# Optimization experiments

Measured on AMD Instinct MI355X. Metric: run time of the kernel, lower is better.

Reference implementation:

```python
import jax, jax.numpy as jnp
import numpy as np

B, S, H = 2, 1024, 4096
NH, NKV, HD = 32, 8, 128
GROUPS = NH // NKV  # num_key_value_groups
ROPE_THETA = 10000.0


def setup_inputs() -> dict:
    key = jax.random.key(0)
    k0, k1, k2 = jax.random.split(key, 3)
    x = jax.random.normal(k0, (B, S, H), jnp.float32)
    w_qkv = jax.random.normal(k1, (H, (NH + 2 * NKV) * HD), jnp.float32) * (1.0 / np.sqrt(H))
    w_o = jax.random.normal(k2, (NH * HD, H), jnp.float32) * (1.0 / np.sqrt(H))
    # rotary cos/sin tables (llama freqs_cis, interleaved-pair convention)
    inv_freq = 1.0 / (ROPE_THETA ** (np.arange(0, HD, 2, dtype=np.float64) / HD))
    freqs = np.outer(np.arange(S, dtype=np.float64), inv_freq)  # [S, HD/2]
    cos = jnp.asarray(np.cos(freqs), jnp.float32)
    sin = jnp.asarray(np.sin(freqs), jnp.float32)
    # additive causal mask [1,1,S,S]
    causal = np.tril(np.ones((S, S), dtype=bool))
    mask = jnp.asarray(np.where(causal, 0.0, -1e9), jnp.float32)[None, None]
    return {"x": x, "w_qkv": w_qkv, "w_o": w_o, "cos": cos, "sin": sin, "mask": mask}


def _rope(t, cos, sin):
    # t: [B,S,N,HD]; rotate interleaved (even, odd) pairs like complex mult by freqs_cis
    t2 = t.reshape(t.shape[:-1] + (HD // 2, 2))
    t0, t1 = t2[..., 0], t2[..., 1]
    c = cos[None, :, None, :]  # [1,S,1,HD/2]
    s = sin[None, :, None, :]
    r0 = t0 * c - t1 * s
    r1 = t0 * s + t1 * c
    return jnp.stack([r0, r1], axis=-1).reshape(t.shape)


def reference(x, w_qkv, w_o, cos, sin, mask):
    b, s, _ = x.shape
    xqkv = (x @ w_qkv).reshape(b, s, NH + 2 * NKV, HD)
    xq = xqkv[:, :, :NH]                  # [b,s,NH,HD]
    xk = xqkv[:, :, NH:NH + NKV]          # [b,s,NKV,HD]
    xv = xqkv[:, :, NH + NKV:]            # [b,s,NKV,HD]
    xq = _rope(xq, cos, sin)
    xk = _rope(xk, cos, sin)
    # GQA: repeat kv heads to match query heads (repeat_interleave on head dim)
    k = jnp.repeat(xk, GROUPS, axis=2)
    v = jnp.repeat(xv, GROUPS, axis=2)
    scores = jnp.einsum('bqhd,bkhd->bhqk', xq, k) / np.float32(np.sqrt(HD))
    scores = scores + mask
    probs = jax.nn.softmax(scores.astype(jnp.float32), axis=-1).astype(xq.dtype)
    out = jnp.einsum('bhqk,bkhd->bqhd', probs, v).reshape(b, s, NH * HD)
    return out @ w_o
```

## Files before the change

kernel.cpp:

```cpp
#include <hip/hip_runtime.h>
#include <cstdint>
#include <cstddef>

typedef short bf16x8 __attribute__((ext_vector_type(8)));
typedef float f32x4 __attribute__((ext_vector_type(4)));

__device__ __forceinline__ unsigned short f2bf(float f) {
  unsigned int u = __builtin_bit_cast(unsigned int, f);
  u += 0x7fffu + ((u >> 16) & 1u);
  return (unsigned short)(u >> 16);
}

__device__ __forceinline__ void transpose_tile(const float* __restrict__ src,
                                               unsigned short* __restrict__ dst,
                                               int K, int N, int n0, int k0, int tid,
                                               float* __restrict__ tb ) {
#pragma unroll
  for (int i = 0; i < 4; ++i) {
    const int lr = tid >> 4, lc = (tid & 15) * 4;
    float4 v = *(const float4*)(src + (size_t)(k0 + i * 16 + lr) * N + n0 + lc);
    tb[(i * 16 + lr) * 65 + lc] = v.x;
    tb[(i * 16 + lr) * 65 + lc + 1] = v.y;
    tb[(i * 16 + lr) * 65 + lc + 2] = v.z;
    tb[(i * 16 + lr) * 65 + lc + 3] = v.w;
  }
  __syncthreads();
  const int nr = tid >> 3, kk = (tid & 7) * 8;
#pragma unroll
  for (int i = 0; i < 2; ++i) {
    int n = nr + i * 32;
    bf16x8 v;
#pragma unroll
    for (int j = 0; j < 8; ++j) v[j] = (short)f2bf(tb[(kk + j) * 65 + n]);
    *(bf16x8*)(dst + (size_t)(n0 + n) * K + k0 + kk) = v;
  }
}

__global__ __launch_bounds__(256) void k_prep(const float* __restrict__ x,
                                              const float* __restrict__ w_qkv,
                                              unsigned short* __restrict__ xb,
                                              unsigned short* __restrict__ wqkv_t) {
  __shared__ float tb[64 * 65];
  const int bid = blockIdx.x, tid = threadIdx.x;
  if (bid < 8192) {
    int i = bid * 256 + tid;
    float4 v = ((const float4*)x)[i];
    ushort4 o;
    o.x = f2bf(v.x); o.y = f2bf(v.y); o.z = f2bf(v.z); o.w = f2bf(v.w);
    ((ushort4*)xb)[i] = o;
  } else {
    int t = bid - 8192;
    transpose_tile(w_qkv, wqkv_t, 4096, 6144, (t % 96) * 64, (t / 96) * 64, tid, tb);
  }
}

template <int MODE>
__global__ __launch_bounds__(256) void k_gemm(const unsigned short* __restrict__ A,
                                              const unsigned short* __restrict__ Bt,
                                              float* __restrict__ C,
                                              unsigned short* __restrict__ Qr,
                                              unsigned short* __restrict__ Kr,
                                              unsigned short* __restrict__ Vt,
                                              const float* __restrict__ cosT,
                                              const float* __restrict__ sinT,
                                              const float* __restrict__ w_o,
                                              unsigned short* __restrict__ wo_t,
                                              int M, int N, int K) {
  __shared__ __align__(16) char smem[32768];
  unsigned short* lA = (unsigned short*)smem;
  unsigned short* lB = (unsigned short*)(smem + 16384);
  const int tid = threadIdx.x;

  int bm, bn;
  if (MODE == 1) {
    const int bid = blockIdx.x;
    if (bid >= 768) {
      int t = bid - 768;
      transpose_tile(w_o, wo_t, 4096, 4096, (t & 63) * 64, (t >> 6) * 64, tid, (float*)smem);
      return;
    }
    const int swz = (bid & 7) * 96 + (bid >> 3);
    bm = (swz & 15) * 128;
    bn = (swz >> 4) * 128;
  } else {
    const int lid = blockIdx.y * gridDim.x + blockIdx.x;
    const int cpx = (gridDim.x * gridDim.y) >> 3;
    const int swz = (lid & 7) * cpx + (lid >> 3);
    bm = (swz % gridDim.x) * 128;
    bn = (swz / gridDim.x) * 128;
  }

  const int lane = tid & 63, wv = tid >> 6;
  const int wr = wv >> 1, wc = wv & 1;
  const int l16 = lane & 15, lhi = lane >> 4;
  f32x4 acc[4][4] = {};
  bf16x8 ar[4], br[4];

#pragma unroll
  for (int i = 0; i < 4; ++i) {
    int c = tid + i * 256, row = c >> 3, c16 = c & 7;
    ar[i] = *(const bf16x8*)(A + (size_t)(bm + row) * K + 0 + c16 * 8);
    br[i] = *(const bf16x8*)(Bt + (size_t)(bn + row) * K + 0 + c16 * 8);
  }
  const int nkt = K >> 6;
  for (int kt = 0; kt < nkt; ++kt) {
    __syncthreads();
#pragma unroll
    for (int i = 0; i < 4; ++i) {
      int c = tid + i * 256, row = c >> 3, c16 = c & 7;
      int pc = c16 ^ (row & 7);
      *(bf16x8*)((char*)lA + row * 128 + pc * 16) = ar[i];
      *(bf16x8*)((char*)lB + row * 128 + pc * 16) = br[i];
    }
    __syncthreads();
    if (kt + 1 < nkt) {
      int kofs = (kt + 1) << 6;
#pragma unroll
      for (int i = 0; i < 4; ++i) {
        int c = tid + i * 256, row = c >> 3, c16 = c & 7;
        ar[i] = *(const bf16x8*)(A + (size_t)(bm + row) * K + kofs + c16 * 8);
        br[i] = *(const bf16x8*)(Bt + (size_t)(bn + row) * K + kofs + c16 * 8);
      }
    }
#pragma unroll
    for (int s = 0; s < 2; ++s) {
      bf16x8 af[4], bfr[4];
#pragma unroll
      for (int f = 0; f < 4; ++f) {
        int rowa = wr * 64 + f * 16 + l16;
        int ca = (s * 4 + lhi) ^ (rowa & 7);
        af[f] = *(const bf16x8*)((char*)lA + rowa * 128 + ca * 16);
        int rowb = wc * 64 + f * 16 + l16;
        int cb = (s * 4 + lhi) ^ (rowb & 7);
        bfr[f] = *(const bf16x8*)((char*)lB + rowb * 128 + cb * 16);
      }
#pragma unroll
      for (int fi = 0; fi < 4; ++fi)
#pragma unroll
        for (int fj = 0; fj < 4; ++fj)
          acc[fi][fj] = __builtin_amdgcn_mfma_f32_16x16x32_bf16(af[fi], bfr[fj], acc[fi][fj], 0, 0, 0);
    }
  }

  if (MODE == 0) {
#pragma unroll
    for (int fi = 0; fi < 4; ++fi) {
      int rbase = bm + wr * 64 + fi * 16 + lhi * 4;
#pragma unroll
      for (int fj = 0; fj < 4; ++fj) {
        int col = bn + wc * 64 + fj * 16 + l16;
#pragma unroll
        for (int r = 0; r < 4; ++r)
          C[(size_t)(rbase + r) * N + col] = acc[fi][fj][r];
      }
    }
  } else {
#pragma unroll
    for (int fi = 0; fi < 4; ++fi) {
      int rbase = bm + wr * 64 + fi * 16 + lhi * 4;
      int b = rbase >> 10, sbase = rbase & 1023;
#pragma unroll
      for (int fj = 0; fj < 4; ++fj) {
        int col = bn + wc * 64 + fj * 16 + l16;
        if (col < 5120) {
          int i = (col & 127) >> 1;
          float sgn = (col & 1) ? 1.0f : -1.0f;
          unsigned short* dst;
          if (col < 4096)
            dst = Qr + ((size_t)(b * 32 + (col >> 7)) * 1024) * 128 + (col & 127);
          else
            dst = Kr + ((size_t)(b * 8 + ((col - 4096) >> 7)) * 1024) * 128 + (col & 127);
#pragma unroll
          for (int r = 0; r < 4; ++r) {
            float own = acc[fi][fj][r];
            float other = __shfl_xor(own, 1);
            int s = sbase + r;
            float c = cosT[s * 64 + i], sn = sinT[s * 64 + i];
            dst[(size_t)s * 128] = f2bf(own * c + sgn * other * sn);
          }
        } else {
          int kvh = (col - 5120) >> 7, d = col & 127;
          unsigned short* dst = Vt + ((size_t)(b * 8 + kvh) * 128 + d) * 1024;
#pragma unroll
          for (int r = 0; r < 4; ++r) dst[sbase + r] = f2bf(acc[fi][fj][r]);
        }
      }
    }
  }
}

__global__ __launch_bounds__(256) void k_attn(const unsigned short* __restrict__ Qr,
                                              const unsigned short* __restrict__ Kr,
                                              const unsigned short* __restrict__ Vt,
                                              unsigned short* __restrict__ Out) {
  __shared__ __align__(16) unsigned short lK[64 * 128];
  __shared__ __align__(16) unsigned short lV[128 * 64];
  __shared__ __align__(16) unsigned short lP[4 * 16 * 64];
  const int tid = threadIdx.x, lane = tid & 63, wv = tid >> 6;
  const int qt = (int)gridDim.x - 1 - (int)blockIdx.x;
  const int h = blockIdx.y, b = blockIdx.z;
  const int kvh = h >> 2;
  const int q0 = qt * 64;
  const int l16 = lane & 15, lhi = lane >> 4;

  const unsigned short* Qbase = Qr + ((size_t)(b * 32 + h) * 1024 + q0 + wv * 16 + l16) * 128;
  bf16x8 qf[4];
#pragma unroll
  for (int s = 0; s < 4; ++s) qf[s] = *(const bf16x8*)(Qbase + s * 32 + lhi * 8);

  const unsigned short* Kbase = Kr + (size_t)(b * 8 + kvh) * 1024 * 128;
  const unsigned short* Vbase = Vt + (size_t)(b * 8 + kvh) * 128 * 1024;

  f32x4 oacc[8] = {};
  float mrow[4] = {-1e30f, -1e30f, -1e30f, -1e30f};
  float lrow[4] = {0.f, 0.f, 0.f, 0.f};
  const int ntk = qt + 1;
  bf16x8 kreg[4], vreg[4];

#pragma unroll
  for (int i = 0; i < 4; ++i) {
    int c = tid + i * 256;
    int krow = c >> 4, kc = c & 15;
    kreg[i] = *(const bf16x8*)(Kbase + (size_t)krow * 128 + kc * 8);
    int vrow = c >> 3, vc = c & 7;
    vreg[i] = *(const bf16x8*)(Vbase + (size_t)vrow * 1024 + vc * 8);
  }

  for (int kt = 0; kt < ntk; ++kt) {
    const int k0 = kt * 64;
    __syncthreads();
#pragma unroll
    for (int i = 0; i < 4; ++i) {
      int c = tid + i * 256;
      int krow = c >> 4, kc = c & 15;
      *(bf16x8*)((char*)lK + krow * 256 + (kc ^ (krow & 7)) * 16) = kreg[i];
      int vrow = c >> 3, vc = c & 7;
      *(bf16x8*)((char*)lV + vrow * 128 + (vc ^ (vrow & 7)) * 16) = vreg[i];
    }
    __syncthreads();

    if (kt + 1 < ntk) {
      const int kn = (kt + 1) * 64;
#pragma unroll
      for (int i = 0; i < 4; ++i) {
        int c = tid + i * 256;
        int krow = c >> 4, kc = c & 15;
        kreg[i] = *(const bf16x8*)(Kbase + (size_t)(kn + krow) * 128 + kc * 8);
        int vrow = c >> 3, vc = c & 7;
        vreg[i] = *(const bf16x8*)(Vbase + (size_t)vrow * 1024 + kn + vc * 8);
      }
    }

    f32x4 sacc[4] = {};
#pragma unroll
    for (int kf = 0; kf < 4; ++kf) {
      int rowk = kf * 16 + l16;
#pragma unroll
      for (int s = 0; s < 4; ++s) {
        int ck = (s * 4 + lhi) ^ (rowk & 7);
        bf16x8 kfr = *(const bf16x8*)((char*)lK + rowk * 256 + ck * 16);
        sacc[kf] = __builtin_amdgcn_mfma_f32_16x16x32_bf16(qf[s], kfr, sacc[kf], 0, 0, 0);
      }
    }

    const int qg = q0 + wv * 16 + lhi * 4;
    float mt[4] = {-1e30f, -1e30f, -1e30f, -1e30f};
#pragma unroll
    for (int kf = 0; kf < 4; ++kf) {
      int kg = k0 + kf * 16 + l16;
#pragma unroll
      for (int r = 0; r < 4; ++r) {
        float v = sacc[kf][r] * 0.08838834764831845f;
        v = (kg <= qg + r) ? v : -1e9f;
        sacc[kf][r] = v;
        mt[r] = fmaxf(mt[r], v);
      }
    }
#pragma unroll
    for (int r = 0; r < 4; ++r) {
#pragma unroll
      for (int off = 1; off < 16; off <<= 1) mt[r] = fmaxf(mt[r], __shfl_xor(mt[r], off));
    }

    bool need = false;
#pragma unroll
    for (int r = 0; r < 4; ++r) need = need || (mt[r] > mrow[r] + 8.0f);
    const bool doresc = (__ballot(need) != 0ull);

    float alpha[4], rs[4];
#pragma unroll
    for (int r = 0; r < 4; ++r) {
      if (doresc) {
        float mn = fmaxf(mrow[r], mt[r]);
        alpha[r] = __expf(mrow[r] - mn);
        mrow[r] = mn;
      } else {
        alpha[r] = 1.0f;
      }
      rs[r] = 0.f;
    }
#pragma unroll
    for (int kf = 0; kf < 4; ++kf) {
      int key = kf * 16 + l16;
#pragma unroll
      for (int r = 0; r < 4; ++r) {
        float p = __expf(sacc[kf][r] - mrow[r]);
        rs[r] += p;
        int prow = lhi * 4 + r;
        int addr = wv * 2048 + ((prow * 128 + key * 2) ^ ((prow & 7) << 4));
        *(unsigned short*)((char*)lP + addr) = f2bf(p);
      }
    }
#pragma unroll
    for (int r = 0; r < 4; ++r) {
#pragma unroll
      for (int off = 1; off < 16; off <<= 1) rs[r] += __shfl_xor(rs[r], off);
      lrow[r] = lrow[r] * alpha[r] + rs[r];
    }
    if (doresc) {
#pragma unroll
      for (int nf = 0; nf < 8; ++nf)
#pragma unroll
        for (int r = 0; r < 4; ++r) oacc[nf][r] *= alpha[r];
    }

#pragma unroll
    for (int s2 = 0; s2 < 2; ++s2) {
      int prow = l16;
      int paddr = wv * 2048 + ((prow * 128 + s2 * 64 + lhi * 16) ^ ((prow & 7) << 4));
      bf16x8 pa = *(const bf16x8*)((char*)lP + paddr);
#pragma unroll
      for (int nf = 0; nf < 8; ++nf) {
        int rowd = nf * 16 + l16;
        int cv = (s2 * 4 + lhi) ^ (rowd & 7);
        bf16x8 vfr = *(const bf16x8*)((char*)lV + rowd * 128 + cv * 16);
        oacc[nf] = __builtin_amdgcn_mfma_f32_16x16x32_bf16(pa, vfr, oacc[nf], 0, 0, 0);
      }
    }
  }

  unsigned short* Ob = Out + ((size_t)(b * 1024) + q0 + wv * 16 + lhi * 4) * 4096 + h * 128;
#pragma unroll
  for (int r = 0; r < 4; ++r) {
    float inv = 1.f / lrow[r];
#pragma unroll
    for (int nf = 0; nf < 8; ++nf)
      Ob[(size_t)r * 4096 + nf * 16 + l16] = f2bf(oacc[nf][r] * inv);
  }
}

extern "C" void kernel_launch(void* const* d_in, const int* in_sizes, int n_in,
                              void* d_out, int out_size, void* d_ws, size_t ws_size,
                              hipStream_t stream) {
  const float* x = (const float*)d_in[0];
  const float* w_qkv = (const float*)d_in[1];
  const float* w_o = (const float*)d_in[2];
  const float* cosT = (const float*)d_in[3];
  const float* sinT = (const float*)d_in[4];

  char* ws = (char*)d_ws;
  unsigned short* wqkv_t = (unsigned short*)(ws);
  unsigned short* wo_t   = (unsigned short*)(ws + 50331648);
  unsigned short* xb     = (unsigned short*)(ws + 83886080);
  unsigned short* Qr     = (unsigned short*)(ws + 100663296);
  unsigned short* Kr     = (unsigned short*)(ws + 117440512);
  unsigned short* Vt     = (unsigned short*)(ws + 121634816);
  unsigned short* attn   = (unsigned short*)(ws + 125829120);

  k_prep<<<14336, 256, 0, stream>>>(x, w_qkv, xb, wqkv_t);
  k_gemm<1><<<768 + 4096, 256, 0, stream>>>(xb, wqkv_t, nullptr, Qr, Kr, Vt, cosT, sinT,
                                            w_o, wo_t, 2048, 6144, 4096);
  k_attn<<<dim3(16, 32, 2), 256, 0, stream>>>(Qr, Kr, Vt, attn);
  k_gemm<0><<<dim3(16, 32), 256, 0, stream>>>(attn, wo_t, (float*)d_out, nullptr, nullptr, nullptr,
                                              nullptr, nullptr, nullptr, nullptr, 2048, 4096, 4096);
}
```

Baseline: 318.8 us.

## Fuse all stages into one cooperative persistent kernel with grid syncs

Replaces the four-kernel pipeline with a single cooperative kernel of 768 blocks. It runs prep, the QKV GEMM with RoPE, attention and the output GEMM in sequence, separated by grid.sync. Attention work is load-balanced by pairing each causal tile with its complement, and the w_o transpose fills the idle blocks during the attention phase. This removes launch gaps and hides the w_o transpose, but adds grid-barrier cost, a per-call host occupancy query and properties lookup, and leaves a third of the blocks idle in the final GEMM. The old multi-kernel path is kept as a fallback.

```diff
diff --git a/kernel.cpp b/kernel.cpp
--- a/kernel.cpp
+++ b/kernel.cpp
@@ -1,6 +1,9 @@
 #include <hip/hip_runtime.h>
+#include <hip/hip_cooperative_groups.h>
 #include <cstdint>
 #include <cstddef>
+
+namespace cg = cooperative_groups;
 
 typedef short bf16x8 __attribute__((ext_vector_type(8)));
 typedef float f32x4 __attribute__((ext_vector_type(4)));
@@ -33,6 +36,353 @@
 #pragma unroll
     for (int j = 0; j < 8; ++j) v[j] = (short)f2bf(tb[(kk + j) * 65 + n]);
     *(bf16x8*)(dst + (size_t)(n0 + n) * K + k0 + kk) = v;
+  }
+}
+
+__device__ __forceinline__ void gemm_core(const unsigned short* __restrict__ A,
+                                          const unsigned short* __restrict__ Bt,
+                                          int K, int bm, int bn, int tid,
+                                          unsigned short* __restrict__ lA,
+                                          unsigned short* __restrict__ lB,
+                                          f32x4 (&acc)[4][4]) {
+  const int lane = tid & 63, wv = tid >> 6;
+  const int wr = wv >> 1, wc = wv & 1;
+  const int l16 = lane & 15, lhi = lane >> 4;
+  bf16x8 ar[4], br[4];
+#pragma unroll
+  for (int i = 0; i < 4; ++i) {
+    int c = tid + i * 256, row = c >> 3, c16 = c & 7;
+    ar[i] = *(const bf16x8*)(A + (size_t)(bm + row) * K + 0 + c16 * 8);
+    br[i] = *(const bf16x8*)(Bt + (size_t)(bn + row) * K + 0 + c16 * 8);
+  }
+  const int nkt = K >> 6;
+  for (int kt = 0; kt < nkt; ++kt) {
+    __syncthreads();
+#pragma unroll
+    for (int i = 0; i < 4; ++i) {
+      int c = tid + i * 256, row = c >> 3, c16 = c & 7;
+      int pc = c16 ^ (row & 7);
+      *(bf16x8*)((char*)lA + row * 128 + pc * 16) = ar[i];
+      *(bf16x8*)((char*)lB + row * 128 + pc * 16) = br[i];
+    }
+    __syncthreads();
+    if (kt + 1 < nkt) {
+      int kofs = (kt + 1) << 6;
+#pragma unroll
+      for (int i = 0; i < 4; ++i) {
+        int c = tid + i * 256, row = c >> 3, c16 = c & 7;
+        ar[i] = *(const bf16x8*)(A + (size_t)(bm + row) * K + kofs + c16 * 8);
+        br[i] = *(const bf16x8*)(Bt + (size_t)(bn + row) * K + kofs + c16 * 8);
+      }
+    }
+#pragma unroll
+    for (int s = 0; s < 2; ++s) {
+      bf16x8 af[4], bfr[4];
+#pragma unroll
+      for (int f = 0; f < 4; ++f) {
+        int rowa = wr * 64 + f * 16 + l16;
+        int ca = (s * 4 + lhi) ^ (rowa & 7);
+        af[f] = *(const bf16x8*)((char*)lA + rowa * 128 + ca * 16);
+        int rowb = wc * 64 + f * 16 + l16;
+        int cb = (s * 4 + lhi) ^ (rowb & 7);
+        bfr[f] = *(const bf16x8*)((char*)lB + rowb * 128 + cb * 16);
+      }
+#pragma unroll
+      for (int fi = 0; fi < 4; ++fi)
+#pragma unroll
+        for (int fj = 0; fj < 4; ++fj)
+          acc[fi][fj] = __builtin_amdgcn_mfma_f32_16x16x32_bf16(af[fi], bfr[fj], acc[fi][fj], 0, 0, 0);
+    }
+  }
+}
+
+__device__ __forceinline__ void qkv_epilogue(f32x4 (&acc)[4][4], int bm, int bn, int tid,
+                                             unsigned short* __restrict__ Qr,
+                                             unsigned short* __restrict__ Kr,
+                                             unsigned short* __restrict__ Vt,
+                                             const float* __restrict__ cosT,
+                                             const float* __restrict__ sinT) {
+  const int lane = tid & 63, wv = tid >> 6;
+  const int wr = wv >> 1, wc = wv & 1;
+  const int l16 = lane & 15, lhi = lane >> 4;
+#pragma unroll
+  for (int fi = 0; fi < 4; ++fi) {
+    int rbase = bm + wr * 64 + fi * 16 + lhi * 4;
+    int b = rbase >> 10, sbase = rbase & 1023;
+#pragma unroll
+    for (int fj = 0; fj < 4; ++fj) {
+      int col = bn + wc * 64 + fj * 16 + l16;
+      if (col < 5120) {
+        int ip = (col & 127) >> 1;
+        float sgn = (col & 1) ? 1.0f : -1.0f;
+        unsigned short* dst;
+        if (col < 4096)
+          dst = Qr + ((size_t)(b * 32 + (col >> 7)) * 1024) * 128 + (col & 127);
+        else
+          dst = Kr + ((size_t)(b * 8 + ((col - 4096) >> 7)) * 1024) * 128 + (col & 127);
+#pragma unroll
+        for (int r = 0; r < 4; ++r) {
+          float own = acc[fi][fj][r];
+          float other = __shfl_xor(own, 1);
+          int s = sbase + r;
+          float c = cosT[s * 64 + ip], sn = sinT[s * 64 + ip];
+          dst[(size_t)s * 128] = f2bf(own * c + sgn * other * sn);
+        }
+      } else {
+        int kvh = (col - 5120) >> 7, d = col & 127;
+        unsigned short* dst = Vt + ((size_t)(b * 8 + kvh) * 128 + d) * 1024;
+#pragma unroll
+        for (int r = 0; r < 4; ++r) dst[sbase + r] = f2bf(acc[fi][fj][r]);
+      }
+    }
+  }
+}
+
+__device__ __forceinline__ void attn_tile(const unsigned short* __restrict__ Qr,
+                                          const unsigned short* __restrict__ Kr,
+                                          const unsigned short* __restrict__ Vt,
+                                          unsigned short* __restrict__ Out,
+                                          int qt, int h, int b, int tid,
+                                          unsigned short* __restrict__ lK,
+                                          unsigned short* __restrict__ lV,
+                                          unsigned short* __restrict__ lP) {
+  const int lane = tid & 63, wv = tid >> 6;
+  const int kvh = h >> 2;
+  const int q0 = qt * 64;
+  const int l16 = lane & 15, lhi = lane >> 4;
+
+  const unsigned short* Qbase = Qr + ((size_t)(b * 32 + h) * 1024 + q0 + wv * 16 + l16) * 128;
+  bf16x8 qf[4];
+#pragma unroll
+  for (int s = 0; s < 4; ++s) qf[s] = *(const bf16x8*)(Qbase + s * 32 + lhi * 8);
+
+  const unsigned short* Kbase = Kr + (size_t)(b * 8 + kvh) * 1024 * 128;
+  const unsigned short* Vbase = Vt + (size_t)(b * 8 + kvh) * 128 * 1024;
+
+  f32x4 oacc[8] = {};
+  float mrow[4] = {-1e30f, -1e30f, -1e30f, -1e30f};
+  float lrow[4] = {0.f, 0.f, 0.f, 0.f};
+  const int ntk = qt + 1;
+  bf16x8 kreg[4], vreg[4];
+
+#pragma unroll
+  for (int i = 0; i < 4; ++i) {
+    int c = tid + i * 256;
+    int krow = c >> 4, kc = c & 15;
+    kreg[i] = *(const bf16x8*)(Kbase + (size_t)krow * 128 + kc * 8);
+    int vrow = c >> 3, vc = c & 7;
+    vreg[i] = *(const bf16x8*)(Vbase + (size_t)vrow * 1024 + vc * 8);
+  }
+
+  for (int kt = 0; kt < ntk; ++kt) {
+    const int k0 = kt * 64;
+    __syncthreads();
+#pragma unroll
+    for (int i = 0; i < 4; ++i) {
+      int c = tid + i * 256;
+      int krow = c >> 4, kc = c & 15;
+      *(bf16x8*)((char*)lK + krow * 256 + (kc ^ (krow & 7)) * 16) = kreg[i];
+      int vrow = c >> 3, vc = c & 7;
+      *(bf16x8*)((char*)lV + vrow * 128 + (vc ^ (vrow & 7)) * 16) = vreg[i];
+    }
+    __syncthreads();
+
+    if (kt + 1 < ntk) {
+      const int kn = (kt + 1) * 64;
+#pragma unroll
+      for (int i = 0; i < 4; ++i) {
+        int c = tid + i * 256;
+        int krow = c >> 4, kc = c & 15;
+        kreg[i] = *(const bf16x8*)(Kbase + (size_t)(kn + krow) * 128 + kc * 8);
+        int vrow = c >> 3, vc = c & 7;
+        vreg[i] = *(const bf16x8*)(Vbase + (size_t)vrow * 1024 + kn + vc * 8);
+      }
+    }
+
+    f32x4 sacc[4] = {};
+#pragma unroll
+    for (int kf = 0; kf < 4; ++kf) {
+      int rowk = kf * 16 + l16;
+#pragma unroll
+      for (int s = 0; s < 4; ++s) {
+        int ck = (s * 4 + lhi) ^ (rowk & 7);
+        bf16x8 kfr = *(const bf16x8*)((char*)lK + rowk * 256 + ck * 16);
+        sacc[kf] = __builtin_amdgcn_mfma_f32_16x16x32_bf16(qf[s], kfr, sacc[kf], 0, 0, 0);
+      }
+    }
+
+    const int qg = q0 + wv * 16 + lhi * 4;
+    float mt[4] = {-1e30f, -1e30f, -1e30f, -1e30f};
+#pragma unroll
+    for (int kf = 0; kf < 4; ++kf) {
+      int kg = k0 + kf * 16 + l16;
+#pragma unroll
+      for (int r = 0; r < 4; ++r) {
+        float v = sacc[kf][r] * 0.08838834764831845f;
+        v = (kg <= qg + r) ? v : -1e9f;
+        sacc[kf][r] = v;
+        mt[r] = fmaxf(mt[r], v);
+      }
+    }
+#pragma unroll
+    for (int r = 0; r < 4; ++r) {
+#pragma unroll
+      for (int off = 1; off < 16; off <<= 1) mt[r] = fmaxf(mt[r], __shfl_xor(mt[r], off));
+    }
+
+    bool need = false;
+#pragma unroll
+    for (int r = 0; r < 4; ++r) need = need || (mt[r] > mrow[r] + 8.0f);
+    const bool doresc = (__ballot(need) != 0ull);
+
+    float alpha[4], rs[4];
+#pragma unroll
+    for (int r = 0; r < 4; ++r) {
+      if (doresc) {
+        float mn = fmaxf(mrow[r], mt[r]);
+        alpha[r] = __expf(mrow[r] - mn);
+        mrow[r] = mn;
+      } else {
+        alpha[r] = 1.0f;
+      }
+      rs[r] = 0.f;
+    }
+#pragma unroll
+    for (int kf = 0; kf < 4; ++kf) {
+      int key = kf * 16 + l16;
+#pragma unroll
+      for (int r = 0; r < 4; ++r) {
+        float p = __expf(sacc[kf][r] - mrow[r]);
+        rs[r] += p;
+        int prow = lhi * 4 + r;
+        int addr = wv * 2048 + ((prow * 128 + key * 2) ^ ((prow & 7) << 4));
+        *(unsigned short*)((char*)lP + addr) = f2bf(p);
+      }
+    }
+#pragma unroll
+    for (int r = 0; r < 4; ++r) {
+#pragma unroll
+      for (int off = 1; off < 16; off <<= 1) rs[r] += __shfl_xor(rs[r], off);
+      lrow[r] = lrow[r] * alpha[r] + rs[r];
+    }
+    if (doresc) {
+#pragma unroll
+      for (int nf = 0; nf < 8; ++nf)
+#pragma unroll
+        for (int r = 0; r < 4; ++r) oacc[nf][r] *= alpha[r];
+    }
+
+#pragma unroll
+    for (int s2 = 0; s2 < 2; ++s2) {
+      int prow = l16;
+      int paddr = wv * 2048 + ((prow * 128 + s2 * 64 + lhi * 16) ^ ((prow & 7) << 4));
+      bf16x8 pa = *(const bf16x8*)((char*)lP + paddr);
+#pragma unroll
+      for (int nf = 0; nf < 8; ++nf) {
+        int rowd = nf * 16 + l16;
+        int cv = (s2 * 4 + lhi) ^ (rowd & 7);
+        bf16x8 vfr = *(const bf16x8*)((char*)lV + rowd * 128 + cv * 16);
+        oacc[nf] = __builtin_amdgcn_mfma_f32_16x16x32_bf16(pa, vfr, oacc[nf], 0, 0, 0);
+      }
+    }
+  }
+
+  unsigned short* Ob = Out + ((size_t)(b * 1024) + q0 + wv * 16 + lhi * 4) * 4096 + h * 128;
+#pragma unroll
+  for (int r = 0; r < 4; ++r) {
+    float inv = 1.f / lrow[r];
+#pragma unroll
+    for (int nf = 0; nf < 8; ++nf)
+      Ob[(size_t)r * 4096 + nf * 16 + l16] = f2bf(oacc[nf][r] * inv);
+  }
+}
+
+__global__ __launch_bounds__(256, 3) void k_mega(
+    const float* __restrict__ x, const float* __restrict__ w_qkv,
+    const float* __restrict__ w_o, const float* __restrict__ cosT,
+    const float* __restrict__ sinT, unsigned short* __restrict__ xb,
+    unsigned short* __restrict__ wqkv_t, unsigned short* __restrict__ wo_t,
+    unsigned short* __restrict__ Qr, unsigned short* __restrict__ Kr,
+    unsigned short* __restrict__ Vt, unsigned short* __restrict__ attnO,
+    float* __restrict__ outp) {
+  __shared__ __align__(16) char smem[40960];
+  cg::grid_group grid = cg::this_grid();
+  const int bid = blockIdx.x, tid = threadIdx.x;
+
+  for (int it = bid; it < 14336; it += 768) {
+    if (it < 8192) {
+      int i = it * 256 + tid;
+      float4 v = ((const float4*)x)[i];
+      ushort4 o;
+      o.x = f2bf(v.x); o.y = f2bf(v.y); o.z = f2bf(v.z); o.w = f2bf(v.w);
+      ((ushort4*)xb)[i] = o;
+    } else {
+      int t = it - 8192;
+      __syncthreads();
+      transpose_tile(w_qkv, wqkv_t, 4096, 6144, (t % 96) * 64, (t / 96) * 64, tid, (float*)smem);
+    }
+  }
+  __threadfence();
+  grid.sync();
+
+  {
+    unsigned short* lA = (unsigned short*)smem;
+    unsigned short* lB = (unsigned short*)(smem + 16384);
+    const int swz = (bid & 7) * 96 + (bid >> 3);
+    const int bm = (swz & 15) * 128, bn = (swz >> 4) * 128;
+    f32x4 acc[4][4] = {};
+    gemm_core(xb, wqkv_t, 4096, bm, bn, tid, lA, lB, acc);
+    qkv_epilogue(acc, bm, bn, tid, Qr, Kr, Vt, cosT, sinT);
+  }
+  __threadfence();
+  grid.sync();
+
+  {
+    unsigned short* lK = (unsigned short*)smem;
+    unsigned short* lV = (unsigned short*)(smem + 16384);
+    unsigned short* lP = (unsigned short*)(smem + 32768);
+    int t1 = bid;
+    attn_tile(Qr, Kr, Vt, attnO, t1 & 15, (t1 >> 4) & 31, t1 >> 9, tid, lK, lV, lP);
+    if (bid < 256) {
+      int t2 = 1023 - bid;
+      attn_tile(Qr, Kr, Vt, attnO, t2 & 15, (t2 >> 4) & 31, t2 >> 9, tid, lK, lV, lP);
+    } else {
+      int g = (bid - 256) >> 4, a = bid & 15;
+      int t0 = g * 136 + 16 * a - (a * (a - 1)) / 2;
+      int cnt = 16 - a;
+      for (int j = 0; j < cnt; ++j) {
+        int t = t0 + j;
+        if (t < 4096) {
+          __syncthreads();
+          transpose_tile(w_o, wo_t, 4096, 4096, (t & 63) * 64, (t >> 6) * 64, tid, (float*)smem);
+        }
+      }
+    }
+  }
+  __threadfence();
+  grid.sync();
+
+  if (bid < 512) {
+    unsigned short* lA = (unsigned short*)smem;
+    unsigned short* lB = (unsigned short*)(smem + 16384);
+    const int swz = (bid & 7) * 64 + (bid >> 3);
+    const int bm = (swz & 15) * 128, bn = (swz >> 4) * 128;
+    f32x4 acc[4][4] = {};
+    gemm_core(attnO, wo_t, 4096, bm, bn, tid, lA, lB, acc);
+    const int lane = tid & 63, wv = tid >> 6;
+    const int wr = wv >> 1, wc = wv & 1;
+    const int l16 = lane & 15, lhi = lane >> 4;
+#pragma unroll
+    for (int fi = 0; fi < 4; ++fi) {
+      int rbase = bm + wr * 64 + fi * 16 + lhi * 4;
+#pragma unroll
+      for (int fj = 0; fj < 4; ++fj) {
+        int col = bn + wc * 64 + fj * 16 + l16;
+#pragma unroll
+        for (int r = 0; r < 4; ++r)
+          outp[(size_t)(rbase + r) * 4096 + col] = acc[fi][fj][r];
+      }
+    }
   }
 }
 
@@ -54,298 +404,68 @@
   }
 }
 
-template <int MODE>
-__global__ __launch_bounds__(256) void k_gemm(const unsigned short* __restrict__ A,
-                                              const unsigned short* __restrict__ Bt,
-                                              float* __restrict__ C,
-                                              unsigned short* __restrict__ Qr,
-                                              unsigned short* __restrict__ Kr,
-                                              unsigned short* __restrict__ Vt,
-                                              const float* __restrict__ cosT,
-                                              const float* __restrict__ sinT,
-                                              const float* __restrict__ w_o,
-                                              unsigned short* __restrict__ wo_t,
-                                              int M, int N, int K) {
+__global__ __launch_bounds__(256) void k_qkv(const unsigned short* __restrict__ A,
+                                             const unsigned short* __restrict__ Bt,
+                                             unsigned short* __restrict__ Qr,
+                                             unsigned short* __restrict__ Kr,
+                                             unsigned short* __restrict__ Vt,
+                                             const float* __restrict__ cosT,
+                                             const float* __restrict__ sinT,
+                                             const float* __restrict__ w_o,
+                                             unsigned short* __restrict__ wo_t) {
+  __shared__ __align__(16) char smem[32768];
+  const int bid = blockIdx.x, tid = threadIdx.x;
+  if (bid >= 768) {
+    int t = bid - 768;
+    transpose_tile(w_o, wo_t, 4096, 4096, (t & 63) * 64, (t >> 6) * 64, tid, (float*)smem);
+    return;
+  }
+  unsigned short* lA = (unsigned short*)smem;
+  unsigned short* lB = (unsigned short*)(smem + 16384);
+  const int swz = (bid & 7) * 96 + (bid >> 3);
+  const int bm = (swz & 15) * 128, bn = (swz >> 4) * 128;
+  f32x4 acc[4][4] = {};
+  gemm_core(A, Bt, 4096, bm, bn, tid, lA, lB, acc);
+  qkv_epilogue(acc, bm, bn, tid, Qr, Kr, Vt, cosT, sinT);
+}
+
+__global__ __launch_bounds__(256) void k_attn(const unsigned short* __restrict__ Qr,
+                                              const unsigned short* __restrict__ Kr,
+                                              const unsigned short* __restrict__ Vt,
+                                              unsigned short* __restrict__ Out) {
+  __shared__ __align__(16) char smem[40960];
+  unsigned short* lK = (unsigned short*)smem;
+  unsigned short* lV = (unsigned short*)(smem + 16384);
+  unsigned short* lP = (unsigned short*)(smem + 32768);
+  const int qt = (int)gridDim.x - 1 - (int)blockIdx.x;
+  attn_tile(Qr, Kr, Vt, Out, qt, blockIdx.y, blockIdx.z, threadIdx.x, lK, lV, lP);
+}
+
+__global__ __launch_bounds__(256) void k_out(const unsigned short* __restrict__ A,
+                                             const unsigned short* __restrict__ Bt,
+                                             float* __restrict__ C) {
   __shared__ __align__(16) char smem[32768];
   unsigned short* lA = (unsigned short*)smem;
   unsigned short* lB = (unsigned short*)(smem + 16384);
   const int tid = threadIdx.x;
-
-  int bm, bn;
-  if (MODE == 1) {
-    const int bid = blockIdx.x;
-    if (bid >= 768) {
-      int t = bid - 768;
-      transpose_tile(w_o, wo_t, 4096, 4096, (t & 63) * 64, (t >> 6) * 64, tid, (float*)smem);
-      return;
-    }
-    const int swz = (bid & 7) * 96 + (bid >> 3);
-    bm = (swz & 15) * 128;
-    bn = (swz >> 4) * 128;
-  } else {
-    const int lid = blockIdx.y * gridDim.x + blockIdx.x;
-    const int cpx = (gridDim.x * gridDim.y) >> 3;
-    const int swz = (lid & 7) * cpx + (lid >> 3);
-    bm = (swz % gridDim.x) * 128;
-    bn = (swz / gridDim.x) * 128;
-  }
-
+  const int lid = blockIdx.y * gridDim.x + blockIdx.x;
+  const int swz = (lid & 7) * 64 + (lid >> 3);
+  const int bm = (swz & 15) * 128, bn = (swz >> 4) * 128;
+  f32x4 acc[4][4] = {};
+  gemm_core(A, Bt, 4096, bm, bn, tid, lA, lB, acc);
   const int lane = tid & 63, wv = tid >> 6;
   const int wr = wv >> 1, wc = wv & 1;
   const int l16 = lane & 15, lhi = lane >> 4;
-  f32x4 acc[4][4] = {};
-  bf16x8 ar[4], br[4];
-
-#pragma unroll
-  for (int i = 0; i < 4; ++i) {
-    int c = tid + i * 256, row = c >> 3, c16 = c & 7;
-    ar[i] = *(const bf16x8*)(A + (size_t)(bm + row) * K + 0 + c16 * 8);
-    br[i] = *(const bf16x8*)(Bt + (size_t)(bn + row) * K + 0 + c16 * 8);
-  }
-  const int nkt = K >> 6;
-  for (int kt = 0; kt < nkt; ++kt) {
-    __syncthreads();
-#pragma unroll
-    for (int i = 0; i < 4; ++i) {
-      int c = tid + i * 256, row = c >> 3, c16 = c & 7;
-      int pc = c16 ^ (row & 7);
-      *(bf16x8*)((char*)lA + row * 128 + pc * 16) = ar[i];
-      *(bf16x8*)((char*)lB + row * 128 + pc * 16) = br[i];
-    }
-    __syncthreads();
-    if (kt + 1 < nkt) {
-      int kofs = (kt + 1) << 6;
-#pragma unroll
-      for (int i = 0; i < 4; ++i) {
-        int c = tid + i * 256, row = c >> 3, c16 = c & 7;
-        ar[i] = *(const bf16x8*)(A + (size_t)(bm + row) * K + kofs + c16 * 8);
-        br[i] = *(const bf16x8*)(Bt + (size_t)(bn + row) * K + kofs + c16 * 8);
-      }
-    }
-#pragma unroll
-    for (int s = 0; s < 2; ++s) {
-      bf16x8 af[4], bfr[4];
-#pragma unroll
-      for (int f = 0; f < 4; ++f) {
-        int rowa = wr * 64 + f * 16 + l16;
-        int ca = (s * 4 + lhi) ^ (rowa & 7);
-        af[f] = *(const bf16x8*)((char*)lA + rowa * 128 + ca * 16);
-        int rowb = wc * 64 + f * 16 + l16;
-        int cb = (s * 4 + lhi) ^ (rowb & 7);
-        bfr[f] = *(const bf16x8*)((char*)lB + rowb * 128 + cb * 16);
-      }
-#pragma unroll
-      for (int fi = 0; fi < 4; ++fi)
-#pragma unroll
-        for (int fj = 0; fj < 4; ++fj)
-          acc[fi][fj] = __builtin_amdgcn_mfma_f32_16x16x32_bf16(af[fi], bfr[fj], acc[fi][fj], 0, 0, 0);
-    }
-  }
-
-  if (MODE == 0) {
-#pragma unroll
-    for (int fi = 0; fi < 4; ++fi) {
-      int rbase = bm + wr * 64 + fi * 16 + lhi * 4;
-#pragma unroll
-      for (int fj = 0; fj < 4; ++fj) {
-        int col = bn + wc * 64 + fj * 16 + l16;
-#pragma unroll
-        for (int r = 0; r < 4; ++r)
-          C[(size_t)(rbase + r) * N + col] = acc[fi][fj][r];
-      }
-    }
-  } else {
-#pragma unroll
-    for (int fi = 0; fi < 4; ++fi) {
-      int rbase = bm + wr * 64 + fi * 16 + lhi * 4;
-      int b = rbase >> 10, sbase = rbase & 1023;
-#pragma unroll
-      for (int fj = 0; fj < 4; ++fj) {
-        int col = bn + wc * 64 + fj * 16 + l16;
-        if (col < 5120) {
-          int i = (col & 127) >> 1;
-          float sgn = (col & 1) ? 1.0f : -1.0f;
-          unsigned short* dst;
-          if (col < 4096)
-            dst = Qr + ((size_t)(b * 32 + (col >> 7)) * 1024) * 128 + (col & 127);
-          else
-            dst = Kr + ((size_t)(b * 8 + ((col - 4096) >> 7)) * 1024) * 128 + (col & 127);
-#pragma unroll
-          for (int r = 0; r < 4; ++r) {
-            float own = acc[fi][fj][r];
-            float other = __shfl_xor(own, 1);
-            int s = sbase + r;
-            float c = cosT[s * 64 + i], sn = sinT[s * 64 + i];
-            dst[(size_t)s * 128] = f2bf(own * c + sgn * other * sn);
-          }
-        } else {
-          int kvh = (col - 5120) >> 7, d = col & 127;
-          unsigned short* dst = Vt + ((size_t)(b * 8 + kvh) * 128 + d) * 1024;
-#pragma unroll
-          for (int r = 0; r < 4; ++r) dst[sbase + r] = f2bf(acc[fi][fj][r]);
-        }
-      }
-    }
-  }
-}
-
-__global__ __launch_bounds__(256) void k_attn(const unsigned short* __restrict__ Qr,
-                                              const unsigned short* __restrict__ Kr,
-                                              const unsigned short* __restrict__ Vt,
-                                              unsigned short* __restrict__ Out) {
-  __shared__ __align__(16) unsigned short lK[64 * 128];
-  __shared__ __align__(16) unsigned short lV[128 * 64];
-  __shared__ __align__(16) unsigned short lP[4 * 16 * 64];
-  const int tid = threadIdx.x, lane = tid & 63, wv = tid >> 6;
-  const int qt = (int)gridDim.x - 1 - (int)blockIdx.x;
-  const int h = blockIdx.y, b = blockIdx.z;
-  const int kvh = h >> 2;
-  const int q0 = qt * 64;
-  const int l16 = lane & 15, lhi = lane >> 4;
-
-  const unsigned short* Qbase = Qr + ((size_t)(b * 32 + h) * 1024 + q0 + wv * 16 + l16) * 128;
-  bf16x8 qf[4];
-#pragma unroll
-  for (int s = 0; s < 4; ++s) qf[s] = *(const bf16x8*)(Qbase + s * 32 + lhi * 8);
-
-  const unsigned short* Kbase = Kr + (size_t)(b * 8 + kvh) * 1024 * 128;
-  const unsigned short* Vbase = Vt + (size_t)(b * 8 + kvh) * 128 * 1024;
-
-  f32x4 oacc[8] = {};
-  float mrow[4] = {-1e30f, -1e30f, -1e30f, -1e30f};
-  float lrow[4] = {0.f, 0.f, 0.f, 0.f};
-  const int ntk = qt + 1;
-  bf16x8 kreg[4], vreg[4];
-
-#pragma unroll
-  for (int i = 0; i < 4; ++i) {
-    int c = tid + i * 256;
-    int krow = c >> 4, kc = c & 15;
-    kreg[i] = *(const bf16x8*)(Kbase + (size_t)krow * 128 + kc * 8);
-    int vrow = c >> 3, vc = c & 7;
-    vreg[i] = *(const bf16x8*)(Vbase + (size_t)vrow * 1024 + vc * 8);
-  }
-
-  for (int kt = 0; kt < ntk; ++kt) {
-    const int k0 = kt * 64;
-    __syncthreads();
-#pragma unroll
-    for (int i = 0; i < 4; ++i) {
-      int c = tid + i * 256;
-      int krow = c >> 4, kc = c & 15;
-      *(bf16x8*)((char*)lK + krow * 256 + (kc ^ (krow & 7)) * 16) = kreg[i];
-      int vrow = c >> 3, vc = c & 7;
-      *(bf16x8*)((char*)lV + vrow * 128 + (vc ^ (vrow & 7)) * 16) = vreg[i];
-    }
-    __syncthreads();
-
-    if (kt + 1 < ntk) {
-      const int kn = (kt + 1) * 64;
-#pragma unroll
-      for (int i = 0; i < 4; ++i) {
-        int c = tid + i * 256;
-        int krow = c >> 4, kc = c & 15;
-        kreg[i] = *(const bf16x8*)(Kbase + (size_t)(kn + krow) * 128 + kc * 8);
-        int vrow = c >> 3, vc = c & 7;
-        vreg[i] = *(const bf16x8*)(Vbase + (size_t)vrow * 1024 + kn + vc * 8);
-      }
-    }
-
-    f32x4 sacc[4] = {};
-#pragma unroll
-    for (int kf = 0; kf < 4; ++kf) {
-      int rowk = kf * 16 + l16;
-#pragma unroll
-      for (int s = 0; s < 4; ++s) {
-        int ck = (s * 4 + lhi) ^ (rowk & 7);
-        bf16x8 kfr = *(const bf16x8*)((char*)lK + rowk * 256 + ck * 16);
-        sacc[kf] = __builtin_amdgcn_mfma_f32_16x16x32_bf16(qf[s], kfr, sacc[kf], 0, 0, 0);
-      }
-    }
-
-    const int qg = q0 + wv * 16 + lhi * 4;
-    float mt[4] = {-1e30f, -1e30f, -1e30f, -1e30f};
-#pragma unroll
-    for (int kf = 0; kf < 4; ++kf) {
-      int kg = k0 + kf * 16 + l16;
-#pragma unroll
-      for (int r = 0; r < 4; ++r) {
-        float v = sacc[kf][r] * 0.08838834764831845f;
-        v = (kg <= qg + r) ? v : -1e9f;
-        sacc[kf][r] = v;
-        mt[r] = fmaxf(mt[r], v);
-      }
-    }
-#pragma unroll
-    for (int r = 0; r < 4; ++r) {
-#pragma unroll
-      for (int off = 1; off < 16; off <<= 1) mt[r] = fmaxf(mt[r], __shfl_xor(mt[r], off));
-    }
-
-    bool need = false;
-#pragma unroll
-    for (int r = 0; r < 4; ++r) need = need || (mt[r] > mrow[r] + 8.0f);
-    const bool doresc = (__ballot(need) != 0ull);
-
-    float alpha[4], rs[4];
-#pragma unroll
-    for (int r = 0; r < 4; ++r) {
-      if (doresc) {
-        float mn = fmaxf(mrow[r], mt[r]);
-        alpha[r] = __expf(mrow[r] - mn);
-        mrow[r] = mn;
-      } else {
-        alpha[r] = 1.0f;
-      }
-      rs[r] = 0.f;
-    }
-#pragma unroll
-    for (int kf = 0; kf < 4; ++kf) {
-      int key = kf * 16 + l16;
-#pragma unroll
-      for (int r = 0; r < 4; ++r) {
-        float p = __expf(sacc[kf][r] - mrow[r]);
-        rs[r] += p;
-        int prow = lhi * 4 + r;
-        int addr = wv * 2048 + ((prow * 128 + key * 2) ^ ((prow & 7) << 4));
-        *(unsigned short*)((char*)lP + addr) = f2bf(p);
-      }
-    }
-#pragma unroll
-    for (int r = 0; r < 4; ++r) {
-#pragma unroll
-      for (int off = 1; off < 16; off <<= 1) rs[r] += __shfl_xor(rs[r], off);
-      lrow[r] = lrow[r] * alpha[r] + rs[r];
-    }
-    if (doresc) {
-#pragma unroll
-      for (int nf = 0; nf < 8; ++nf)
-#pragma unroll
-        for (int r = 0; r < 4; ++r) oacc[nf][r] *= alpha[r];
-    }
-
-#pragma unroll
-    for (int s2 = 0; s2 < 2; ++s2) {
-      int prow = l16;
-      int paddr = wv * 2048 + ((prow * 128 + s2 * 64 + lhi * 16) ^ ((prow & 7) << 4));
-      bf16x8 pa = *(const bf16x8*)((char*)lP + paddr);
-#pragma unroll
-      for (int nf = 0; nf < 8; ++nf) {
-        int rowd = nf * 16 + l16;
-        int cv = (s2 * 4 + lhi) ^ (rowd & 7);
-        bf16x8 vfr = *(const bf16x8*)((char*)lV + rowd * 128 + cv * 16);
-        oacc[nf] = __builtin_amdgcn_mfma_f32_16x16x32_bf16(pa, vfr, oacc[nf], 0, 0, 0);
-      }
-    }
-  }
-
-  unsigned short* Ob = Out + ((size_t)(b * 1024) + q0 + wv * 16 + lhi * 4) * 4096 + h * 128;
-#pragma unroll
-  for (int r = 0; r < 4; ++r) {
-    float inv = 1.f / lrow[r];
-#pragma unroll
-    for (int nf = 0; nf < 8; ++nf)
-      Ob[(size_t)r * 4096 + nf * 16 + l16] = f2bf(oacc[nf][r] * inv);
+#pragma unroll
+  for (int fi = 0; fi < 4; ++fi) {
+    int rbase = bm + wr * 64 + fi * 16 + lhi * 4;
+#pragma unroll
+    for (int fj = 0; fj < 4; ++fj) {
+      int col = bn + wc * 64 + fj * 16 + l16;
+#pragma unroll
+      for (int r = 0; r < 4; ++r)
+        C[(size_t)(rbase + r) * 4096 + col] = acc[fi][fj][r];
+    }
   }
 }
 
@@ -366,11 +486,26 @@
   unsigned short* Kr     = (unsigned short*)(ws + 117440512);
   unsigned short* Vt     = (unsigned short*)(ws + 121634816);
   unsigned short* attn   = (unsigned short*)(ws + 125829120);
+  float* outp = (float*)d_out;
+
+  int dev = 0;
+  hipGetDevice(&dev);
+  hipDeviceProp_t prop;
+  hipGetDeviceProperties(&prop, dev);
+  int nb = 0;
+  hipOccupancyMaxActiveBlocksPerMultiprocessor(&nb, k_mega, 256, 0);
+  bool coop = (prop.cooperativeLaunch != 0) && (nb * prop.multiProcessorCount >= 768);
+
+  if (coop) {
+    void* args[] = {&x, &w_qkv, &w_o, &cosT, &sinT, &xb, &wqkv_t, &wo_t,
+                    &Qr, &Kr, &Vt, &attn, &outp};
+    hipError_t e = hipLaunchCooperativeKernel((const void*)k_mega, dim3(768), dim3(256),
+                                              args, 0, stream);
+    if (e == hipSuccess) return;
+  }
 
   k_prep<<<14336, 256, 0, stream>>>(x, w_qkv, xb, wqkv_t);
-  k_gemm<1><<<768 + 4096, 256, 0, stream>>>(xb, wqkv_t, nullptr, Qr, Kr, Vt, cosT, sinT,
-                                            w_o, wo_t, 2048, 6144, 4096);
+  k_qkv<<<768 + 4096, 256, 0, stream>>>(xb, wqkv_t, Qr, Kr, Vt, cosT, sinT, w_o, wo_t);
   k_attn<<<dim3(16, 32, 2), 256, 0, stream>>>(Qr, Kr, Vt, attn);
-  k_gemm<0><<<dim3(16, 32), 256, 0, stream>>>(attn, wo_t, (float*)d_out, nullptr, nullptr, nullptr,
-                                              nullptr, nullptr, nullptr, nullptr, 2048, 4096, 4096);
-}
+  k_out<<<dim3(16, 32), 256, 0, stream>>>(attn, wo_t, outp);
+}
```

New measurement: 345.1 us. +8.2%, slower.
